# Kernel optimization log

Hardware: AMD Instinct MI355X
Metric: run time of the kernel (lower is better)

## Reference

```python
import jax, jax.numpy as jnp
import numpy as np

N_NODES = 100000
N_EDGES = 320000
HID = 256
NE = 128  # node_embed_dim = hid // 2 (use_stats=True, sgrl=False)
N_LAYERS = 3

NET, DEV, PIN = 0, 1, 2


def setup_inputs() -> dict:
    key = jax.random.key(0)
    ks = jax.random.split(key, 24)
    s = 0.05
    inp = {
        "node_attr": jax.random.uniform(ks[0], (N_NODES, 17), dtype=jnp.float32),
        "y": jax.random.uniform(ks[1], (N_NODES, 2), dtype=jnp.float32),
        "node_emb": jax.random.normal(ks[2], (4, NE), dtype=jnp.float32) * s,
        "edge_emb": jax.random.normal(ks[3], (4, HID), dtype=jnp.float32) * s,
        "net_W": jax.random.normal(ks[4], (17, NE), dtype=jnp.float32) * s,
        "net_b": jnp.zeros((NE,), jnp.float32),
        "dev_W": jax.random.normal(ks[5], (17, NE), dtype=jnp.float32) * s,
        "dev_b": jnp.zeros((NE,), jnp.float32),
        "pin_emb": jax.random.normal(ks[6], (17, NE), dtype=jnp.float32) * s,
        "sage_Wl": jax.random.normal(ks[7], (N_LAYERS, HID, HID), dtype=jnp.float32) * s,
        "sage_bl": jnp.zeros((N_LAYERS, HID), jnp.float32),
        "sage_Wr": jax.random.normal(ks[8], (N_LAYERS, HID, HID), dtype=jnp.float32) * s,
        "head_W0": jax.random.normal(ks[9], (HID, HID), dtype=jnp.float32) * s,
        "head_b0": jnp.zeros((HID,), jnp.float32),
        "head_W1": jax.random.normal(ks[10], (HID, 1), dtype=jnp.float32) * s,
        "head_b1": jnp.zeros((1,), jnp.float32),
        "node_type": jax.random.randint(ks[11], (N_NODES,), 0, 4, dtype=jnp.int32),
        "edge_type": jax.random.randint(ks[12], (N_EDGES,), 0, 4, dtype=jnp.int32),
        "edge_index": jax.random.randint(ks[13], (2, N_EDGES), 0, N_NODES, dtype=jnp.int32),
    }
    return inp


def _forward(node_attr, y, node_emb, edge_emb, net_W, net_b, dev_W, dev_b,
             pin_emb, sage_Wl, sage_bl, sage_Wr, head_W0, head_b0, head_W1,
             head_b1, node_type, edge_type, edge_index):
    # node / edge type encoders (embedding lookups)
    x = node_emb[node_type]                 # [N, NE]
    xe = edge_emb[edge_type]                # [N_E, HID] (unused by SAGE, kept for fidelity)
    del xe

    # per-type attribute embedding, scattered into a zero tensor via disjoint masks
    net_mask = node_type == NET
    dev_mask = node_type == DEV
    pin_mask = node_type == PIN
    net_e = node_attr @ net_W + net_b       # [N, NE]
    dev_e = node_attr @ dev_W + dev_b       # [N, NE]
    pin_idx = node_attr[:, 0].astype(jnp.int32)
    pin_e = pin_emb[pin_idx]                # [N, NE]
    attr_emb = jnp.where(net_mask[:, None], net_e,
                jnp.where(dev_mask[:, None], dev_e,
                jnp.where(pin_mask[:, None], pin_e, jnp.zeros_like(net_e))))
    x = jnp.concatenate([x, attr_emb], axis=1)  # [N, HID]

    src, dst = edge_index[0], edge_index[1]
    cnt = jax.ops.segment_sum(jnp.ones_like(src, dtype=x.dtype), dst,
                              num_segments=N_NODES)
    denom = jnp.maximum(cnt, 1.0)[:, None]
    for l in range(N_LAYERS):
        # SAGEConv: mean-aggregate neighbor features, then two linear maps
        agg = jax.ops.segment_sum(x[src], dst, num_segments=N_NODES) / denom
        x = agg @ sage_Wl[l] + sage_bl[l] + x @ sage_Wr[l]
        x = jax.nn.relu(x)

    # head MLP (2 layers): Linear -> ReLU -> Linear
    h = jax.nn.relu(x @ head_W0 + head_b0)
    pred = h @ head_W1 + head_b1            # [N, 1]
    true_class = y[:, 1].astype(jnp.int32)
    true_label = y
    return pred, true_class, true_label


def reference(node_attr, y, node_emb, edge_emb, net_W, net_b, dev_W, dev_b,
              pin_emb, sage_Wl, sage_bl, sage_Wr, head_W0, head_b0, head_W1,
              head_b1, node_type, edge_type, edge_index):
    return _forward(node_attr, y, node_emb, edge_emb, net_W, net_b, dev_W,
                    dev_b, pin_emb, sage_Wl, sage_bl, sage_Wr, head_W0,
                    head_b0, head_W1, head_b1, node_type, edge_type,
                    edge_index)
```

## Files before the change

kernel.cpp:

```cpp
#include <hip/hip_runtime.h>
#include <hip/hip_bf16.h>

#define N_NODES 100000
#define N_EDGES 320000
#define HID 256
#define NE 128
#define NLAYERS 3

typedef __attribute__((ext_vector_type(8))) short short8;
typedef __attribute__((ext_vector_type(4))) float f32x4;

__device__ inline float bfbits2f(unsigned int b) { return __uint_as_float(b << 16); }

__device__ inline unsigned int pack_bf2(float lo, float hi) {
    __hip_bfloat16 l = __float2bfloat16(lo), h = __float2bfloat16(hi);
    return (unsigned int)*(unsigned short*)&l |
           ((unsigned int)*(unsigned short*)&h << 16);
}

__global__ __launch_bounds__(256) void k_prep(
    const float* __restrict__ Wl, const float* __restrict__ Wr,
    const float* __restrict__ W0,
    __hip_bfloat16* __restrict__ Wt, __hip_bfloat16* __restrict__ Wh,
    int* __restrict__ deg, int* __restrict__ total)
{
    int t = blockIdx.x * 256 + threadIdx.x;
    const int total_sage = 3 * 256 * 512;
    if (t < total_sage) {
        int l = t >> 17;
        int rem = t & 131071;
        int n = rem >> 9;
        int k = rem & 511;
        const float* Wsrc = (k < 256) ? (Wl + (size_t)l * 65536)
                                      : (Wr + (size_t)l * 65536);
        Wt[t] = __float2bfloat16(Wsrc[(k & 255) * 256 + n]);
    } else {
        int u = t - total_sage;
        if (u < 65536) {
            int n = u >> 8, k = u & 255;
            Wh[u] = __float2bfloat16(W0[k * 256 + n]);
        }
    }
    if (t < N_NODES) deg[t] = 0;
    if (t == 0) *total = 0;
}

__global__ __launch_bounds__(256) void k_init(
    const float* __restrict__ node_attr,
    const float* __restrict__ node_emb,
    const float* __restrict__ net_W, const float* __restrict__ net_b,
    const float* __restrict__ dev_W, const float* __restrict__ dev_b,
    const float* __restrict__ pin_emb,
    const int*   __restrict__ node_type,
    const float* __restrict__ y, const float* __restrict__ b1,
    float* __restrict__ out,
    __hip_bfloat16* __restrict__ x)
{
    int t = blockIdx.x * 256 + threadIdx.x;
    if (t < N_NODES * 32) {
        int n  = t >> 5;
        int c4 = (t & 31) * 4;
        int ty = node_type[n];
        float4 e = *(const float4*)(node_emb + ty * NE + c4);
        float4 a;
        if (ty == 0 || ty == 1) {
            const float* W = (ty == 0) ? net_W : dev_W;
            const float* b = (ty == 0) ? net_b : dev_b;
            a = *(const float4*)(b + c4);
            const float* ar = node_attr + (size_t)n * 17;
            #pragma unroll
            for (int k = 0; k < 17; ++k) {
                float av = ar[k];
                float4 wv = *(const float4*)(W + k * NE + c4);
                a.x += av * wv.x; a.y += av * wv.y;
                a.z += av * wv.z; a.w += av * wv.w;
            }
        } else if (ty == 2) {
            int idx = (int)node_attr[(size_t)n * 17];
            a = *(const float4*)(pin_emb + idx * NE + c4);
        } else {
            a.x = a.y = a.z = a.w = 0.0f;
        }
        uint2 ev = {pack_bf2(e.x, e.y), pack_bf2(e.z, e.w)};
        uint2 av = {pack_bf2(a.x, a.y), pack_bf2(a.z, a.w)};
        *(uint2*)((char*)x + (size_t)n * 512 + c4 * 2)       = ev;
        *(uint2*)((char*)x + (size_t)n * 512 + 256 + c4 * 2) = av;
    } else {
        int n = t - N_NODES * 32;
        if (n < N_NODES) {
            float y0 = y[(size_t)n * 2 + 0];
            float y1 = y[(size_t)n * 2 + 1];
            out[n] = b1[0];
            out[N_NODES + n] = (float)(int)y1;
            out[2 * N_NODES + 2 * n + 0] = y0;
            out[2 * N_NODES + 2 * n + 1] = y1;
        }
    }
}

__global__ __launch_bounds__(256) void k_hist(
    const int* __restrict__ edge_index, int* __restrict__ deg)
{
    int e = blockIdx.x * 256 + threadIdx.x;
    if (e < N_EDGES) atomicAdd(&deg[edge_index[N_EDGES + e]], 1);
}

__global__ __launch_bounds__(256) void k_alloc(
    const int* __restrict__ deg, int* __restrict__ off,
    int* __restrict__ cursor, int* __restrict__ total)
{
    int n = blockIdx.x * 256 + threadIdx.x;
    int lane = threadIdx.x & 63;
    int d = (n < N_NODES) ? deg[n] : 0;
    int incl = d;
    #pragma unroll
    for (int o = 1; o < 64; o <<= 1) {
        int v = __shfl_up(incl, o, 64);
        if (lane >= o) incl += v;
    }
    int wtot = __shfl(incl, 63, 64);
    int base = 0;
    if (lane == 63) base = atomicAdd(total, wtot);
    base = __shfl(base, 63, 64);
    if (n < N_NODES) {
        int o = base + incl - d;
        off[n] = o;
        cursor[n] = o;
    }
}

__global__ __launch_bounds__(256) void k_fill(
    const int* __restrict__ edge_index, int* __restrict__ cursor,
    int* __restrict__ slots)
{
    int e = blockIdx.x * 256 + threadIdx.x;
    if (e >= N_EDGES) return;
    int s = edge_index[e];
    int d = edge_index[N_EDGES + e];
    int slot = atomicAdd(&cursor[d], 1);
    slots[slot] = s;
}

__global__ __launch_bounds__(256) void k_aggregate(
    const __hip_bfloat16* __restrict__ x,
    const int* __restrict__ off, const int* __restrict__ deg,
    const int* __restrict__ slots,
    __hip_bfloat16* __restrict__ agg)
{
    int g = blockIdx.x * 256 + threadIdx.x;
    int wid = g >> 6;
    int lane = g & 63;
    int sub = lane >> 4;
    int l16 = lane & 15;
    int n = wid * 4 + sub;
    bool active = n < N_NODES;
    int o = 0, d = 0;
    if (active) { o = off[n]; d = deg[n]; }
    float acc[16];
    #pragma unroll
    for (int i = 0; i < 16; ++i) acc[i] = 0.0f;
    for (int p = 0; p < d; ++p) {
        int src = slots[o + p];
        const char* rp = (const char*)x + (size_t)src * 512 + l16 * 32;
        uint4 v0 = *(const uint4*)rp;
        uint4 v1 = *(const uint4*)(rp + 16);
        const unsigned int u[8] = {v0.x, v0.y, v0.z, v0.w, v1.x, v1.y, v1.z, v1.w};
        #pragma unroll
        for (int i = 0; i < 8; ++i) {
            acc[2 * i + 0] += bfbits2f(u[i] & 0xffffu);
            acc[2 * i + 1] += __uint_as_float(u[i] & 0xffff0000u);
        }
    }
    if (active) {
        float rs = 1.0f / fmaxf((float)d, 1.0f);
        unsigned int w[8];
        #pragma unroll
        for (int i = 0; i < 8; ++i)
            w[i] = pack_bf2(acc[2 * i + 0] * rs, acc[2 * i + 1] * rs);
        uint4 o0 = {w[0], w[1], w[2], w[3]};
        uint4 o1 = {w[4], w[5], w[6], w[7]};
        char* op = (char*)agg + (size_t)n * 512 + l16 * 32;
        *(uint4*)op = o0;
        *(uint4*)(op + 16) = o1;
    }
}

template <bool SAGE>
__global__ __launch_bounds__(512, 4) void k_mfma(
    const __hip_bfloat16* __restrict__ Agg,
    const __hip_bfloat16* __restrict__ X,
    const __hip_bfloat16* __restrict__ Wt,
    const float* __restrict__ bias,
    const float* __restrict__ W1,
    __hip_bfloat16* __restrict__ Out,
    float* __restrict__ Pred)
{
    __shared__ char As[2][16384];

    const int tid  = threadIdx.x;
    const int w    = tid >> 6, lane = tid & 63;
    const int l15  = lane & 15, lg = lane >> 4;
    const int row0 = blockIdx.x * 128;
    const int KT     = SAGE ? 512 : 256;
    const int nsteps = SAGE ? 8 : 4;

    f32x4 acc[8][2];
    #pragma unroll
    for (int i = 0; i < 8; ++i)
        #pragma unroll
        for (int n = 0; n < 2; ++n) acc[i][n] = (f32x4)0.0f;

    const int srow   = tid >> 3;
    const int schunk = tid & 7;

    auto stage = [&](int s, int b) {
        const char* base;
        int k0;
        if (SAGE && s < 4) { base = (const char*)Agg; k0 = s * 64; }
        else               { base = (const char*)X;   k0 = (SAGE ? s - 4 : s) * 64; }
        #pragma unroll
        for (int issue = 0; issue < 2; ++issue) {
            int row  = srow + issue * 64;
            int grow = row0 + row;
            if (grow >= N_NODES) grow = N_NODES - 1;
            const char* gp = base + (size_t)grow * 512 + (size_t)k0 * 2
                           + ((schunk ^ (row & 7)) << 4);
            const char* lp = &As[b][issue * 8192 + tid * 16];
            __builtin_amdgcn_global_load_lds(
                (const __attribute__((address_space(1))) void*)gp,
                (__attribute__((address_space(3))) void*)lp, 16, 0, 0);
        }
    };

    auto loadB = [&](int s, short8 (&bb)[2][2]) {
        #pragma unroll
        for (int h = 0; h < 2; ++h)
            #pragma unroll
            for (int n = 0; n < 2; ++n) {
                int c = w * 32 + n * 16 + l15;
                bb[h][n] = *(const short8*)(Wt + (size_t)c * KT + s * 64 + h * 32 + 8 * lg);
            }
    };

    auto do_step = [&](int s, bool last, short8 (&bcur)[2][2], short8 (&bnxt)[2][2]) {
        const int b = s & 1;
        if (last) asm volatile("s_waitcnt vmcnt(0)" ::: "memory");
        else      asm volatile("s_waitcnt vmcnt(2)" ::: "memory");
        __builtin_amdgcn_sched_barrier(0);
        __builtin_amdgcn_s_barrier();
        __builtin_amdgcn_sched_barrier(0);
        if (!last) loadB(s + 1, bnxt);
        #pragma unroll
        for (int h = 0; h < 2; ++h) {
            #pragma unroll
            for (int i = 0; i < 8; ++i) {
                int r = i * 16 + l15;
                short8 a = *(const short8*)&As[b][r * 128 + (((lg + 4 * h) ^ (r & 7)) << 4)];
                acc[i][0] = __builtin_amdgcn_mfma_f32_16x16x32_bf16(a, bcur[h][0], acc[i][0], 0, 0, 0);
                acc[i][1] = __builtin_amdgcn_mfma_f32_16x16x32_bf16(a, bcur[h][1], acc[i][1], 0, 0, 0);
            }
        }
        __builtin_amdgcn_sched_barrier(0);
        __builtin_amdgcn_s_barrier();
        __builtin_amdgcn_sched_barrier(0);
        if (s + 2 < nsteps) stage(s + 2, b);
    };

    short8 b0[2][2], b1[2][2];
    loadB(0, b0);
    stage(0, 0);
    stage(1, 1);
    #pragma unroll
    for (int s = 0; s < nsteps; s += 2) {
        do_step(s,     s == nsteps - 1, b0, b1);
        do_step(s + 1, s + 1 == nsteps - 1, b1, b0);
    }

    if (SAGE) {
        __hip_bfloat16* lo = (__hip_bfloat16*)As;
        #pragma unroll
        for (int hh = 0; hh < 2; ++hh) {
            #pragma unroll
            for (int n = 0; n < 2; ++n) {
                int c = w * 32 + n * 16 + l15;
                float bv = bias[c];
                #pragma unroll
                for (int i2 = 0; i2 < 4; ++i2) {
                    int i = hh * 4 + i2;
                    #pragma unroll
                    for (int r = 0; r < 4; ++r) {
                        int rl = i2 * 16 + lg * 4 + r;
                        lo[rl * 256 + c] = __float2bfloat16(fmaxf(acc[i][n][r] + bv, 0.0f));
                    }
                }
            }
            __syncthreads();
            #pragma unroll
            for (int q = 0; q < 4; ++q) {
                int chunk = tid + q * 512;
                int rl = chunk >> 5, cc = chunk & 31;
                int grow = row0 + hh * 64 + rl;
                if (grow < N_NODES)
                    *(uint4*)((char*)Out + (size_t)grow * 512 + cc * 16) =
                        *(const uint4*)((const char*)As + rl * 512 + cc * 16);
            }
            __syncthreads();
        }
    } else {
        #pragma unroll
        for (int i = 0; i < 8; ++i) {
            float p[4];
            #pragma unroll
            for (int r = 0; r < 4; ++r) p[r] = 0.0f;
            #pragma unroll
            for (int n = 0; n < 2; ++n) {
                int c = w * 32 + n * 16 + l15;
                float bv = bias[c];
                float wv = W1[c];
                #pragma unroll
                for (int r = 0; r < 4; ++r)
                    p[r] += fmaxf(acc[i][n][r] + bv, 0.0f) * wv;
            }
            #pragma unroll
            for (int r = 0; r < 4; ++r) {
                float s = p[r];
                #pragma unroll
                for (int m = 1; m < 16; m <<= 1) s += __shfl_xor(s, m, 64);
                if (l15 == 0) {
                    int row = row0 + i * 16 + lg * 4 + r;
                    if (row < N_NODES) atomicAdd(&Pred[row], s);
                }
            }
        }
    }
}

extern "C" void kernel_launch(void* const* d_in, const int* in_sizes, int n_in,
                              void* d_out, int out_size, void* d_ws, size_t ws_size,
                              hipStream_t stream) {
    const float* node_attr = (const float*)d_in[0];
    const float* y         = (const float*)d_in[1];
    const float* node_emb  = (const float*)d_in[2];
    const float* net_W     = (const float*)d_in[4];
    const float* net_b     = (const float*)d_in[5];
    const float* dev_W     = (const float*)d_in[6];
    const float* dev_b     = (const float*)d_in[7];
    const float* pin_emb   = (const float*)d_in[8];
    const float* sage_Wl   = (const float*)d_in[9];
    const float* sage_bl   = (const float*)d_in[10];
    const float* sage_Wr   = (const float*)d_in[11];
    const float* head_W0   = (const float*)d_in[12];
    const float* head_b0   = (const float*)d_in[13];
    const float* head_W1   = (const float*)d_in[14];
    const float* head_b1   = (const float*)d_in[15];
    const int*   node_type = (const int*)d_in[16];
    const int*   edge_idx  = (const int*)d_in[18];
    float* out = (float*)d_out;

    const size_t xelems = (size_t)N_NODES * HID;
    char* p = (char*)d_ws;
    __hip_bfloat16* x0  = (__hip_bfloat16*)p;  p += xelems * 2;
    __hip_bfloat16* x1  = (__hip_bfloat16*)p;  p += xelems * 2;
    __hip_bfloat16* agg = (__hip_bfloat16*)p;  p += xelems * 2;
    __hip_bfloat16* Wt  = (__hip_bfloat16*)p;  p += (size_t)3 * 256 * 512 * 2;
    __hip_bfloat16* Wh  = (__hip_bfloat16*)p;  p += (size_t)256 * 256 * 2;
    int* deg    = (int*)p; p += N_NODES * 4;
    int* off    = (int*)p; p += N_NODES * 4;
    int* cursor = (int*)p; p += N_NODES * 4;
    int* slots  = (int*)p; p += N_EDGES * 4;
    int* total  = (int*)p; p += 16;

    k_prep<<<(3 * 131072 + 65536 + 255) / 256, 256, 0, stream>>>(
        sage_Wl, sage_Wr, head_W0, Wt, Wh, deg, total);
    k_init<<<(N_NODES * 33 + 255) / 256, 256, 0, stream>>>(
        node_attr, node_emb, net_W, net_b, dev_W, dev_b, pin_emb, node_type,
        y, head_b1, out, x0);
    k_hist<<<(N_EDGES + 255) / 256, 256, 0, stream>>>(edge_idx, deg);
    k_alloc<<<(N_NODES + 255) / 256, 256, 0, stream>>>(deg, off, cursor, total);
    k_fill<<<(N_EDGES + 255) / 256, 256, 0, stream>>>(edge_idx, cursor, slots);

    const int gemm_grid = (N_NODES + 127) / 128;
    __hip_bfloat16* xcur = x0;
    __hip_bfloat16* xalt = x1;
    for (int l = 0; l < NLAYERS; ++l) {
        k_aggregate<<<(N_NODES / 4 * 64 + 255) / 256, 256, 0, stream>>>(
            xcur, off, deg, slots, agg);
        k_mfma<true><<<gemm_grid, 512, 0, stream>>>(
            agg, xcur, Wt + (size_t)l * 131072,
            sage_bl + (size_t)l * HID, nullptr, xalt, nullptr);
        __hip_bfloat16* t = xcur; xcur = xalt; xalt = t;
    }
    k_mfma<false><<<gemm_grid, 512, 0, stream>>>(
        xcur, xcur, Wh, head_b0, head_W1, nullptr, out);
}
```

Measured before the change: 360.1 us.

## Switch SAGE layers to FP8 storage and MFMA, triple-buffer staging, fuse histogram

Node features, aggregates and SAGE weights are now stored as FP8 e4m3, and the SAGE GEMMs use the fp8 MFMA, which halves the gather and GEMM memory traffic. The last SAGE layer writes bf16 for a separate head kernel that keeps the bf16 MFMA. The GEMM pipelines move to a 3-stage LDS ring with a single barrier per step, and the degree histogram is folded into the init kernel to save a launch. FP8 cuts mantissa precision heavily, so accuracy against the fp32 reference may degrade.

```diff
diff --git a/kernel.cpp b/kernel.cpp
--- a/kernel.cpp
+++ b/kernel.cpp
@@ -1,27 +1,29 @@
 #include <hip/hip_runtime.h>
 #include <hip/hip_bf16.h>
+#include <hip/hip_fp8.h>
 
 #define N_NODES 100000
 #define N_EDGES 320000
 #define HID 256
 #define NE 128
-#define NLAYERS 3
 
 typedef __attribute__((ext_vector_type(8))) short short8;
 typedef __attribute__((ext_vector_type(4))) float f32x4;
-
-__device__ inline float bfbits2f(unsigned int b) { return __uint_as_float(b << 16); }
-
-__device__ inline unsigned int pack_bf2(float lo, float hi) {
-    __hip_bfloat16 l = __float2bfloat16(lo), h = __float2bfloat16(hi);
-    return (unsigned int)*(unsigned short*)&l |
-           ((unsigned int)*(unsigned short*)&h << 16);
+typedef long long i64v;
+
+__device__ inline unsigned char f2fp8(float f) { return __hip_fp8_e4m3(f).__x; }
+__device__ inline float fp82f(unsigned char b) {
+    __hip_fp8_e4m3 h; h.__x = b; return (float)h;
+}
+__device__ inline unsigned int pack_fp8x4(float a, float b, float c, float d) {
+    return (unsigned)f2fp8(a) | ((unsigned)f2fp8(b) << 8) |
+           ((unsigned)f2fp8(c) << 16) | ((unsigned)f2fp8(d) << 24);
 }
 
 __global__ __launch_bounds__(256) void k_prep(
     const float* __restrict__ Wl, const float* __restrict__ Wr,
     const float* __restrict__ W0,
-    __hip_bfloat16* __restrict__ Wt, __hip_bfloat16* __restrict__ Wh,
+    unsigned char* __restrict__ Wt8, __hip_bfloat16* __restrict__ Wh,
     int* __restrict__ deg, int* __restrict__ total)
 {
     int t = blockIdx.x * 256 + threadIdx.x;
@@ -33,7 +35,7 @@
         int k = rem & 511;
         const float* Wsrc = (k < 256) ? (Wl + (size_t)l * 65536)
                                       : (Wr + (size_t)l * 65536);
-        Wt[t] = __float2bfloat16(Wsrc[(k & 255) * 256 + n]);
+        Wt8[t] = f2fp8(Wsrc[(k & 255) * 256 + n]);
     } else {
         int u = t - total_sage;
         if (u < 65536) {
@@ -53,56 +55,60 @@
     const float* __restrict__ pin_emb,
     const int*   __restrict__ node_type,
     const float* __restrict__ y, const float* __restrict__ b1,
+    const int*   __restrict__ edge_index, int* __restrict__ deg,
     float* __restrict__ out,
-    __hip_bfloat16* __restrict__ x)
+    unsigned char* __restrict__ x)
 {
     int t = blockIdx.x * 256 + threadIdx.x;
-    if (t < N_NODES * 32) {
-        int n  = t >> 5;
-        int c4 = (t & 31) * 4;
+    if (t < N_NODES * 16) {
+        int n  = t >> 4;
+        int c8 = (t & 15) * 8;
         int ty = node_type[n];
-        float4 e = *(const float4*)(node_emb + ty * NE + c4);
-        float4 a;
+        float4 e0 = *(const float4*)(node_emb + ty * NE + c8);
+        float4 e1 = *(const float4*)(node_emb + ty * NE + c8 + 4);
+        float4 a0, a1;
         if (ty == 0 || ty == 1) {
             const float* W = (ty == 0) ? net_W : dev_W;
             const float* b = (ty == 0) ? net_b : dev_b;
-            a = *(const float4*)(b + c4);
+            a0 = *(const float4*)(b + c8);
+            a1 = *(const float4*)(b + c8 + 4);
             const float* ar = node_attr + (size_t)n * 17;
             #pragma unroll
             for (int k = 0; k < 17; ++k) {
                 float av = ar[k];
-                float4 wv = *(const float4*)(W + k * NE + c4);
-                a.x += av * wv.x; a.y += av * wv.y;
-                a.z += av * wv.z; a.w += av * wv.w;
+                float4 w0 = *(const float4*)(W + k * NE + c8);
+                float4 w1 = *(const float4*)(W + k * NE + c8 + 4);
+                a0.x += av * w0.x; a0.y += av * w0.y;
+                a0.z += av * w0.z; a0.w += av * w0.w;
+                a1.x += av * w1.x; a1.y += av * w1.y;
+                a1.z += av * w1.z; a1.w += av * w1.w;
             }
         } else if (ty == 2) {
             int idx = (int)node_attr[(size_t)n * 17];
-            a = *(const float4*)(pin_emb + idx * NE + c4);
+            a0 = *(const float4*)(pin_emb + idx * NE + c8);
+            a1 = *(const float4*)(pin_emb + idx * NE + c8 + 4);
         } else {
-            a.x = a.y = a.z = a.w = 0.0f;
-        }
-        uint2 ev = {pack_bf2(e.x, e.y), pack_bf2(e.z, e.w)};
-        uint2 av = {pack_bf2(a.x, a.y), pack_bf2(a.z, a.w)};
-        *(uint2*)((char*)x + (size_t)n * 512 + c4 * 2)       = ev;
-        *(uint2*)((char*)x + (size_t)n * 512 + 256 + c4 * 2) = av;
+            a0.x = a0.y = a0.z = a0.w = 0.0f;
+            a1 = a0;
+        }
+        uint2 ev = {pack_fp8x4(e0.x, e0.y, e0.z, e0.w),
+                    pack_fp8x4(e1.x, e1.y, e1.z, e1.w)};
+        uint2 av = {pack_fp8x4(a0.x, a0.y, a0.z, a0.w),
+                    pack_fp8x4(a1.x, a1.y, a1.z, a1.w)};
+        *(uint2*)(x + (size_t)n * 256 + c8)       = ev;
+        *(uint2*)(x + (size_t)n * 256 + 128 + c8) = av;
+    } else if (t < N_NODES * 17) {
+        int n = t - N_NODES * 16;
+        float y0 = y[(size_t)n * 2 + 0];
+        float y1 = y[(size_t)n * 2 + 1];
+        out[n] = b1[0];
+        out[N_NODES + n] = (float)(int)y1;
+        out[2 * N_NODES + 2 * n + 0] = y0;
+        out[2 * N_NODES + 2 * n + 1] = y1;
     } else {
-        int n = t - N_NODES * 32;
-        if (n < N_NODES) {
-            float y0 = y[(size_t)n * 2 + 0];
-            float y1 = y[(size_t)n * 2 + 1];
-            out[n] = b1[0];
-            out[N_NODES + n] = (float)(int)y1;
-            out[2 * N_NODES + 2 * n + 0] = y0;
-            out[2 * N_NODES + 2 * n + 1] = y1;
-        }
-    }
-}
-
-__global__ __launch_bounds__(256) void k_hist(
-    const int* __restrict__ edge_index, int* __restrict__ deg)
-{
-    int e = blockIdx.x * 256 + threadIdx.x;
-    if (e < N_EDGES) atomicAdd(&deg[edge_index[N_EDGES + e]], 1);
+        int e = t - N_NODES * 17;
+        if (e < N_EDGES) atomicAdd(&deg[edge_index[N_EDGES + e]], 1);
+    }
 }
 
 __global__ __launch_bounds__(256) void k_alloc(
@@ -142,10 +148,10 @@
 }
 
 __global__ __launch_bounds__(256) void k_aggregate(
-    const __hip_bfloat16* __restrict__ x,
+    const unsigned char* __restrict__ x,
     const int* __restrict__ off, const int* __restrict__ deg,
     const int* __restrict__ slots,
-    __hip_bfloat16* __restrict__ agg)
+    unsigned char* __restrict__ agg)
 {
     int g = blockIdx.x * 256 + threadIdx.x;
     int wid = g >> 6;
@@ -161,48 +167,39 @@
     for (int i = 0; i < 16; ++i) acc[i] = 0.0f;
     for (int p = 0; p < d; ++p) {
         int src = slots[o + p];
-        const char* rp = (const char*)x + (size_t)src * 512 + l16 * 32;
-        uint4 v0 = *(const uint4*)rp;
-        uint4 v1 = *(const uint4*)(rp + 16);
-        const unsigned int u[8] = {v0.x, v0.y, v0.z, v0.w, v1.x, v1.y, v1.z, v1.w};
-        #pragma unroll
-        for (int i = 0; i < 8; ++i) {
-            acc[2 * i + 0] += bfbits2f(u[i] & 0xffffu);
-            acc[2 * i + 1] += __uint_as_float(u[i] & 0xffff0000u);
-        }
+        uint4 v = *(const uint4*)(x + (size_t)src * 256 + l16 * 16);
+        unsigned int uu[4] = {v.x, v.y, v.z, v.w};
+        #pragma unroll
+        for (int j = 0; j < 4; ++j)
+            #pragma unroll
+            for (int b = 0; b < 4; ++b)
+                acc[j * 4 + b] += fp82f((uu[j] >> (8 * b)) & 0xffu);
     }
     if (active) {
         float rs = 1.0f / fmaxf((float)d, 1.0f);
-        unsigned int w[8];
-        #pragma unroll
-        for (int i = 0; i < 8; ++i)
-            w[i] = pack_bf2(acc[2 * i + 0] * rs, acc[2 * i + 1] * rs);
-        uint4 o0 = {w[0], w[1], w[2], w[3]};
-        uint4 o1 = {w[4], w[5], w[6], w[7]};
-        char* op = (char*)agg + (size_t)n * 512 + l16 * 32;
-        *(uint4*)op = o0;
-        *(uint4*)(op + 16) = o1;
-    }
-}
-
-template <bool SAGE>
-__global__ __launch_bounds__(512, 4) void k_mfma(
-    const __hip_bfloat16* __restrict__ Agg,
-    const __hip_bfloat16* __restrict__ X,
-    const __hip_bfloat16* __restrict__ Wt,
+        uint4 ov;
+        ov.x = pack_fp8x4(acc[0] * rs,  acc[1] * rs,  acc[2] * rs,  acc[3] * rs);
+        ov.y = pack_fp8x4(acc[4] * rs,  acc[5] * rs,  acc[6] * rs,  acc[7] * rs);
+        ov.z = pack_fp8x4(acc[8] * rs,  acc[9] * rs,  acc[10] * rs, acc[11] * rs);
+        ov.w = pack_fp8x4(acc[12] * rs, acc[13] * rs, acc[14] * rs, acc[15] * rs);
+        *(uint4*)(agg + (size_t)n * 256 + l16 * 16) = ov;
+    }
+}
+
+template <bool BF16OUT>
+__global__ __launch_bounds__(512, 4) void k_sage(
+    const unsigned char* __restrict__ Agg8,
+    const unsigned char* __restrict__ X8,
+    const unsigned char* __restrict__ Wt8,
     const float* __restrict__ bias,
-    const float* __restrict__ W1,
-    __hip_bfloat16* __restrict__ Out,
-    float* __restrict__ Pred)
-{
-    __shared__ char As[2][16384];
+    void* __restrict__ OutP)
+{
+    __shared__ char smem[32768];
 
     const int tid  = threadIdx.x;
     const int w    = tid >> 6, lane = tid & 63;
     const int l15  = lane & 15, lg = lane >> 4;
     const int row0 = blockIdx.x * 128;
-    const int KT     = SAGE ? 512 : 256;
-    const int nsteps = SAGE ? 8 : 4;
 
     f32x4 acc[8][2];
     #pragma unroll
@@ -210,74 +207,75 @@
         #pragma unroll
         for (int n = 0; n < 2; ++n) acc[i][n] = (f32x4)0.0f;
 
-    const int srow   = tid >> 3;
-    const int schunk = tid & 7;
-
-    auto stage = [&](int s, int b) {
-        const char* base;
-        int k0;
-        if (SAGE && s < 4) { base = (const char*)Agg; k0 = s * 64; }
-        else               { base = (const char*)X;   k0 = (SAGE ? s - 4 : s) * 64; }
-        #pragma unroll
-        for (int issue = 0; issue < 2; ++issue) {
-            int row  = srow + issue * 64;
-            int grow = row0 + row;
-            if (grow >= N_NODES) grow = N_NODES - 1;
-            const char* gp = base + (size_t)grow * 512 + (size_t)k0 * 2
-                           + ((schunk ^ (row & 7)) << 4);
-            const char* lp = &As[b][issue * 8192 + tid * 16];
-            __builtin_amdgcn_global_load_lds(
-                (const __attribute__((address_space(1))) void*)gp,
-                (__attribute__((address_space(3))) void*)lp, 16, 0, 0);
-        }
+    const int srow = tid >> 2;
+    const int c16s = tid & 3;
+    int sgrow = row0 + srow; if (sgrow >= N_NODES) sgrow = N_NODES - 1;
+
+    auto stage = [&](int s) {
+        const int b = s % 3;
+        const unsigned char* base = (s < 4) ? Agg8 : X8;
+        int k0 = (s & 3) * 64;
+        const unsigned char* gp = base + (size_t)sgrow * 256 + k0
+                                + ((c16s ^ (srow & 3)) << 4);
+        const char* lp = smem + b * 8192 + tid * 16;
+        __builtin_amdgcn_global_load_lds(
+            (const __attribute__((address_space(1))) void*)gp,
+            (__attribute__((address_space(3))) void*)lp, 16, 0, 0);
     };
 
-    auto loadB = [&](int s, short8 (&bb)[2][2]) {
+    auto loadB = [&](int s, i64v (&bb)[2][2]) {
         #pragma unroll
         for (int h = 0; h < 2; ++h)
             #pragma unroll
             for (int n = 0; n < 2; ++n) {
                 int c = w * 32 + n * 16 + l15;
-                bb[h][n] = *(const short8*)(Wt + (size_t)c * KT + s * 64 + h * 32 + 8 * lg);
+                bb[h][n] = *(const i64v*)(Wt8 + (size_t)c * 512 + s * 64
+                                          + h * 32 + lg * 8);
             }
     };
 
-    auto do_step = [&](int s, bool last, short8 (&bcur)[2][2], short8 (&bnxt)[2][2]) {
-        const int b = s & 1;
+    auto do_step = [&](int s, bool last, i64v (&bcur)[2][2], i64v (&bnxt)[2][2]) {
+        const int b = s % 3;
         if (last) asm volatile("s_waitcnt vmcnt(0)" ::: "memory");
-        else      asm volatile("s_waitcnt vmcnt(2)" ::: "memory");
+        else      asm volatile("s_waitcnt vmcnt(1)" ::: "memory");
         __builtin_amdgcn_sched_barrier(0);
         __builtin_amdgcn_s_barrier();
         __builtin_amdgcn_sched_barrier(0);
         if (!last) loadB(s + 1, bnxt);
+        if (s + 2 < 8) stage(s + 2);
         #pragma unroll
         for (int h = 0; h < 2; ++h) {
+            const int c8 = h * 4 + lg;
             #pragma unroll
             for (int i = 0; i < 8; ++i) {
                 int r = i * 16 + l15;
-                short8 a = *(const short8*)&As[b][r * 128 + (((lg + 4 * h) ^ (r & 7)) << 4)];
-                acc[i][0] = __builtin_amdgcn_mfma_f32_16x16x32_bf16(a, bcur[h][0], acc[i][0], 0, 0, 0);
-                acc[i][1] = __builtin_amdgcn_mfma_f32_16x16x32_bf16(a, bcur[h][1], acc[i][1], 0, 0, 0);
-            }
-        }
-        __builtin_amdgcn_sched_barrier(0);
-        __builtin_amdgcn_s_barrier();
-        __builtin_amdgcn_sched_barrier(0);
-        if (s + 2 < nsteps) stage(s + 2, b);
+                i64v a = *(const i64v*)(smem + b * 8192 + r * 64
+                            + ((((c8 >> 1) ^ (r & 3)) << 4) | ((c8 & 1) << 3)));
+                acc[i][0] = __builtin_amdgcn_mfma_f32_16x16x32_fp8_fp8(
+                    a, bcur[h][0], acc[i][0], 0, 0, 0);
+                acc[i][1] = __builtin_amdgcn_mfma_f32_16x16x32_fp8_fp8(
+                    a, bcur[h][1], acc[i][1], 0, 0, 0);
+            }
+        }
     };
 
-    short8 b0[2][2], b1[2][2];
+    i64v b0[2][2], b1r[2][2];
     loadB(0, b0);
-    stage(0, 0);
-    stage(1, 1);
-    #pragma unroll
-    for (int s = 0; s < nsteps; s += 2) {
-        do_step(s,     s == nsteps - 1, b0, b1);
-        do_step(s + 1, s + 1 == nsteps - 1, b1, b0);
-    }
-
-    if (SAGE) {
-        __hip_bfloat16* lo = (__hip_bfloat16*)As;
+    stage(0);
+    stage(1);
+    do_step(0, false, b0, b1r);
+    do_step(1, false, b1r, b0);
+    do_step(2, false, b0, b1r);
+    do_step(3, false, b1r, b0);
+    do_step(4, false, b0, b1r);
+    do_step(5, false, b1r, b0);
+    do_step(6, false, b0, b1r);
+    do_step(7, true,  b1r, b0);
+
+    __syncthreads();
+    if (BF16OUT) {
+        __hip_bfloat16* Out = (__hip_bfloat16*)OutP;
+        __hip_bfloat16* lo = (__hip_bfloat16*)smem;
         #pragma unroll
         for (int hh = 0; hh < 2; ++hh) {
             #pragma unroll
@@ -290,7 +288,8 @@
                     #pragma unroll
                     for (int r = 0; r < 4; ++r) {
                         int rl = i2 * 16 + lg * 4 + r;
-                        lo[rl * 256 + c] = __float2bfloat16(fmaxf(acc[i][n][r] + bv, 0.0f));
+                        lo[rl * 256 + c] =
+                            __float2bfloat16(fmaxf(acc[i][n][r] + bv, 0.0f));
                     }
                 }
             }
@@ -302,34 +301,149 @@
                 int grow = row0 + hh * 64 + rl;
                 if (grow < N_NODES)
                     *(uint4*)((char*)Out + (size_t)grow * 512 + cc * 16) =
-                        *(const uint4*)((const char*)As + rl * 512 + cc * 16);
+                        *(const uint4*)((const char*)smem + rl * 512 + cc * 16);
             }
             __syncthreads();
         }
     } else {
-        #pragma unroll
-        for (int i = 0; i < 8; ++i) {
-            float p[4];
-            #pragma unroll
-            for (int r = 0; r < 4; ++r) p[r] = 0.0f;
+        unsigned char* Out = (unsigned char*)OutP;
+        unsigned char* lo = (unsigned char*)smem;
+        #pragma unroll
+        for (int hh = 0; hh < 2; ++hh) {
             #pragma unroll
             for (int n = 0; n < 2; ++n) {
                 int c = w * 32 + n * 16 + l15;
                 float bv = bias[c];
-                float wv = W1[c];
                 #pragma unroll
-                for (int r = 0; r < 4; ++r)
-                    p[r] += fmaxf(acc[i][n][r] + bv, 0.0f) * wv;
-            }
-            #pragma unroll
-            for (int r = 0; r < 4; ++r) {
-                float s = p[r];
-                #pragma unroll
-                for (int m = 1; m < 16; m <<= 1) s += __shfl_xor(s, m, 64);
-                if (l15 == 0) {
-                    int row = row0 + i * 16 + lg * 4 + r;
-                    if (row < N_NODES) atomicAdd(&Pred[row], s);
+                for (int i2 = 0; i2 < 4; ++i2) {
+                    int i = hh * 4 + i2;
+                    #pragma unroll
+                    for (int r = 0; r < 4; ++r) {
+                        int rl = i2 * 16 + lg * 4 + r;
+                        lo[rl * 256 + c] = f2fp8(fmaxf(acc[i][n][r] + bv, 0.0f));
+                    }
                 }
+            }
+            __syncthreads();
+            #pragma unroll
+            for (int q = 0; q < 2; ++q) {
+                int chunk = tid + q * 512;
+                int rl = chunk >> 4, cc = chunk & 15;
+                int grow = row0 + hh * 64 + rl;
+                if (grow < N_NODES)
+                    *(uint4*)(Out + (size_t)grow * 256 + cc * 16) =
+                        *(const uint4*)((const char*)smem + rl * 256 + cc * 16);
+            }
+            __syncthreads();
+        }
+    }
+}
+
+__global__ __launch_bounds__(512, 4) void k_head(
+    const __hip_bfloat16* __restrict__ X,
+    const __hip_bfloat16* __restrict__ Wt,
+    const float* __restrict__ bias,
+    const float* __restrict__ W1,
+    float* __restrict__ Pred)
+{
+    __shared__ char smem[49152];
+
+    const int tid  = threadIdx.x;
+    const int w    = tid >> 6, lane = tid & 63;
+    const int l15  = lane & 15, lg = lane >> 4;
+    const int row0 = blockIdx.x * 128;
+
+    f32x4 acc[8][2];
+    #pragma unroll
+    for (int i = 0; i < 8; ++i)
+        #pragma unroll
+        for (int n = 0; n < 2; ++n) acc[i][n] = (f32x4)0.0f;
+
+    const int srow   = tid >> 3;
+    const int schunk = tid & 7;
+
+    auto stage = [&](int s) {
+        const int b = s % 3;
+        #pragma unroll
+        for (int issue = 0; issue < 2; ++issue) {
+            int row  = srow + issue * 64;
+            int grow = row0 + row;
+            if (grow >= N_NODES) grow = N_NODES - 1;
+            const char* gp = (const char*)X + (size_t)grow * 512 + s * 128
+                           + ((schunk ^ (row & 7)) << 4);
+            const char* lp = smem + b * 16384 + issue * 8192 + tid * 16;
+            __builtin_amdgcn_global_load_lds(
+                (const __attribute__((address_space(1))) void*)gp,
+                (__attribute__((address_space(3))) void*)lp, 16, 0, 0);
+        }
+    };
+
+    auto loadB = [&](int s, short8 (&bb)[2][2]) {
+        #pragma unroll
+        for (int h = 0; h < 2; ++h)
+            #pragma unroll
+            for (int n = 0; n < 2; ++n) {
+                int c = w * 32 + n * 16 + l15;
+                bb[h][n] = *(const short8*)(Wt + (size_t)c * 256 + s * 64
+                                            + h * 32 + 8 * lg);
+            }
+    };
+
+    auto do_step = [&](int s, bool last, short8 (&bcur)[2][2], short8 (&bnxt)[2][2]) {
+        const int b = s % 3;
+        if (last) asm volatile("s_waitcnt vmcnt(0)" ::: "memory");
+        else      asm volatile("s_waitcnt vmcnt(2)" ::: "memory");
+        __builtin_amdgcn_sched_barrier(0);
+        __builtin_amdgcn_s_barrier();
+        __builtin_amdgcn_sched_barrier(0);
+        if (!last) loadB(s + 1, bnxt);
+        if (s + 2 < 4) stage(s + 2);
+        #pragma unroll
+        for (int h = 0; h < 2; ++h) {
+            #pragma unroll
+            for (int i = 0; i < 8; ++i) {
+                int r = i * 16 + l15;
+                short8 a = *(const short8*)(smem + b * 16384 + r * 128
+                                + (((lg + 4 * h) ^ (r & 7)) << 4));
+                acc[i][0] = __builtin_amdgcn_mfma_f32_16x16x32_bf16(
+                    a, bcur[h][0], acc[i][0], 0, 0, 0);
+                acc[i][1] = __builtin_amdgcn_mfma_f32_16x16x32_bf16(
+                    a, bcur[h][1], acc[i][1], 0, 0, 0);
+            }
+        }
+    };
+
+    short8 b0[2][2], b1r[2][2];
+    loadB(0, b0);
+    stage(0);
+    stage(1);
+    do_step(0, false, b0, b1r);
+    do_step(1, false, b1r, b0);
+    do_step(2, false, b0, b1r);
+    do_step(3, true,  b1r, b0);
+
+    #pragma unroll
+    for (int i = 0; i < 8; ++i) {
+        float p[4];
+        #pragma unroll
+        for (int r = 0; r < 4; ++r) p[r] = 0.0f;
+        #pragma unroll
+        for (int n = 0; n < 2; ++n) {
+            int cg = w * 32 + n * 16 + l15;
+            float bv = bias[cg];
+            float wv = W1[cg];
+            #pragma unroll
+            for (int r = 0; r < 4; ++r)
+                p[r] += fmaxf(acc[i][n][r] + bv, 0.0f) * wv;
+        }
+        #pragma unroll
+        for (int r = 0; r < 4; ++r) {
+            float s = p[r];
+            #pragma unroll
+            for (int m = 1; m < 16; m <<= 1) s += __shfl_xor(s, m, 64);
+            if (l15 == 0) {
+                int row = row0 + i * 16 + lg * 4 + r;
+                if (row < N_NODES) atomicAdd(&Pred[row], s);
             }
         }
     }
@@ -357,13 +471,14 @@
     const int*   edge_idx  = (const int*)d_in[18];
     float* out = (float*)d_out;
 
-    const size_t xelems = (size_t)N_NODES * HID;
+    const size_t x8b = (size_t)N_NODES * 256;
     char* p = (char*)d_ws;
-    __hip_bfloat16* x0  = (__hip_bfloat16*)p;  p += xelems * 2;
-    __hip_bfloat16* x1  = (__hip_bfloat16*)p;  p += xelems * 2;
-    __hip_bfloat16* agg = (__hip_bfloat16*)p;  p += xelems * 2;
-    __hip_bfloat16* Wt  = (__hip_bfloat16*)p;  p += (size_t)3 * 256 * 512 * 2;
-    __hip_bfloat16* Wh  = (__hip_bfloat16*)p;  p += (size_t)256 * 256 * 2;
+    unsigned char* x0   = (unsigned char*)p;  p += x8b;
+    unsigned char* x1   = (unsigned char*)p;  p += x8b;
+    unsigned char* agg8 = (unsigned char*)p;  p += x8b;
+    __hip_bfloat16* x3bf = (__hip_bfloat16*)p; p += (size_t)N_NODES * 512;
+    unsigned char* Wt8  = (unsigned char*)p;  p += (size_t)3 * 256 * 512;
+    __hip_bfloat16* Wh  = (__hip_bfloat16*)p; p += (size_t)256 * 256 * 2;
     int* deg    = (int*)p; p += N_NODES * 4;
     int* off    = (int*)p; p += N_NODES * 4;
     int* cursor = (int*)p; p += N_NODES * 4;
@@ -371,25 +486,23 @@
     int* total  = (int*)p; p += 16;
 
     k_prep<<<(3 * 131072 + 65536 + 255) / 256, 256, 0, stream>>>(
-        sage_Wl, sage_Wr, head_W0, Wt, Wh, deg, total);
-    k_init<<<(N_NODES * 33 + 255) / 256, 256, 0, stream>>>(
+        sage_Wl, sage_Wr, head_W0, Wt8, Wh, deg, total);
+    k_init<<<(N_NODES * 17 + N_EDGES + 255) / 256, 256, 0, stream>>>(
         node_attr, node_emb, net_W, net_b, dev_W, dev_b, pin_emb, node_type,
-        y, head_b1, out, x0);
-    k_hist<<<(N_EDGES + 255) / 256, 256, 0, stream>>>(edge_idx, deg);
+        y, head_b1, edge_idx, deg, out, x0);
     k_alloc<<<(N_NODES + 255) / 256, 256, 0, stream>>>(deg, off, cursor, total);
     k_fill<<<(N_EDGES + 255) / 256, 256, 0, stream>>>(edge_idx, cursor, slots);
 
+    const int agg_grid  = (N_NODES / 4 * 64 + 255) / 256;
     const int gemm_grid = (N_NODES + 127) / 128;
-    __hip_bfloat16* xcur = x0;
-    __hip_bfloat16* xalt = x1;
-    for (int l = 0; l < NLAYERS; ++l) {
-        k_aggregate<<<(N_NODES / 4 * 64 + 255) / 256, 256, 0, stream>>>(
-            xcur, off, deg, slots, agg);
-        k_mfma<true><<<gemm_grid, 512, 0, stream>>>(
-            agg, xcur, Wt + (size_t)l * 131072,
-            sage_bl + (size_t)l * HID, nullptr, xalt, nullptr);
-        __hip_bfloat16* t = xcur; xcur = xalt; xalt = t;
-    }
-    k_mfma<false><<<gemm_grid, 512, 0, stream>>>(
-        xcur, xcur, Wh, head_b0, head_W1, nullptr, out);
-}
+    k_aggregate<<<agg_grid, 256, 0, stream>>>(x0, off, deg, slots, agg8);
+    k_sage<false><<<gemm_grid, 512, 0, stream>>>(
+        agg8, x0, Wt8, sage_bl, x1);
+    k_aggregate<<<agg_grid, 256, 0, stream>>>(x1, off, deg, slots, agg8);
+    k_sage<false><<<gemm_grid, 512, 0, stream>>>(
+        agg8, x1, Wt8 + 131072, sage_bl + HID, x0);
+    k_aggregate<<<agg_grid, 256, 0, stream>>>(x0, off, deg, slots, agg8);
+    k_sage<true><<<gemm_grid, 512, 0, stream>>>(
+        agg8, x0, Wt8 + 262144, sage_bl + 2 * HID, x3bf);
+    k_head<<<gemm_grid, 512, 0, stream>>>(x3bf, Wh, head_b0, head_W1, out);
+}
```

New measurement: 359.8 us. Within noise of the previous version (-0.1%).
